# Kernel optimization log

Hardware: AMD Instinct MI355X
Metric: run time of the kernel (lower is better)

The kernel has to match this reference:

```python
import jax, jax.numpy as jnp
import numpy as np

X_CH, Y_CH = 3, 31
C = X_CH + Y_CH            # s_channels = m_channels = 34
A = C * (C - 1) // 2       # 561 Givens rotation angles
SMIN, SMAX = 0.001, 1000.0


def setup_inputs() -> dict:
    key = jax.random.key(0)
    k1, k2 = jax.random.split(key)
    x = jax.random.normal(k1, (4, X_CH, 64, 64), dtype=jnp.float32)
    W = jax.random.normal(k2, (C + C + A, X_CH), dtype=jnp.float32) * 0.1
    b = jnp.zeros((C + C + A,), dtype=jnp.float32)
    return {"x": x, "W": W, "b": b}


def _covariance(s, a):
    # s: (B, C, H, W) positive variances; a: (B, A, H, W) rotation angles.
    B, _, H, Wd = s.shape
    cs = jnp.moveaxis(jnp.cos(a), 1, 0)  # (A, B, H, W)
    ss = jnp.moveaxis(jnp.sin(a), 1, 0)  # (A, B, H, W)
    ii, jj = np.triu_indices(C, k=1)      # same (i, j) order as the torch double loop
    ii = jnp.asarray(ii, dtype=jnp.int32)
    jj = jnp.asarray(jj, dtype=jnp.int32)

    # R starts as identity; each Givens rotation rij only mixes columns i and j
    # of R (R <- R @ rij), so we update two columns instead of a full matmul.
    R0 = jnp.broadcast_to(jnp.eye(C, dtype=s.dtype), (B, H, Wd, C, C))

    def step(R, inp):
        c_, s_, i, j = inp
        col_i = R[..., i]                      # (B, H, W, C)
        col_j = R[..., j]
        c_ = c_[..., None]
        s_ = s_[..., None]
        R = R.at[..., i].set(c_ * col_i + s_ * col_j)
        R = R.at[..., j].set(-s_ * col_i + c_ * col_j)
        return R, None

    R, _ = jax.lax.scan(step, R0, (cs, ss, ii, jj))
    sp = jnp.transpose(s, (0, 2, 3, 1))        # (B, H, W, C)
    # S = R^T D R with D = diag(sp): S[k,n] = sum_m R[m,k] * sp[m] * R[m,n]
    S = jnp.einsum('bhwmk,bhwm,bhwmn->bhwkn', R, sp, R)
    D = jnp.zeros((B, H, Wd, C, C), dtype=s.dtype).at[..., jnp.arange(C), jnp.arange(C)].set(sp)
    return S, R, D


def reference(x, W, b):
    # 1x1-conv encoder: (B, 3, H, W) -> (B, 629, H, W)
    w = jnp.einsum('oc,bchw->bohw', W, x) + b[None, :, None, None]
    m = jnp.transpose(w[:, :C], (0, 2, 3, 1))                  # (B, H, W, C) mean
    s = jax.nn.sigmoid(w[:, C:2 * C])
    s = SMIN * (1.0 - s) + SMAX * s                            # (B, C, H, W)
    a = jnp.pi * jnp.tanh(w[:, 2 * C:])                        # (B, A, H, W)
    S, _, _ = _covariance(s, a)
    return m, S, s
```

## Files before the change

### kernel.cpp

```cpp
#include <hip/hip_runtime.h>


#define CCH 34
#define ACH 561
#define HWPIX 4096
#define NPIX 16384
#define PXB 6
#define NPRB 3
#define NTHR 128
#define CSPP (141 * 16)
#define CBUF (NPRB * CSPP)
#define VROW 36
#define VPX (17 * VROW * 4)
#define OFF_S 557056
#define OFF_s 19496960
#define LOG2E 1.4426950408889634f

typedef float    f32x2 __attribute__((ext_vector_type(2)));
typedef _Float16 h2    __attribute__((ext_vector_type(2)));

struct Pairs {
    short i[ACH]; short j[ACH];
    constexpr Pairs() : i(), j() {
        int p = 0;
        for (int a = 0; a < CCH - 1; ++a)
            for (int b = a + 1; b < CCH; ++b) { i[p] = (short)a; j[p] = (short)b; ++p; }
    }
};
__device__ constexpr Pairs PR{};

__device__ __forceinline__ float dot2h(h2 a, h2 b, float c) {
#if __has_builtin(__builtin_amdgcn_fdot2)
    return __builtin_amdgcn_fdot2(a, b, c, false);
#else
    return fmaf((float)a[0], (float)b[0], fmaf((float)a[1], (float)b[1], c));
#endif
}

__device__ __forceinline__ void rot2(f32x2& Ri, f32x2& Rj, f32x2 c2, f32x2 s2) {
    f32x2 t1 = s2 * Rj;
    f32x2 t2 = s2 * Ri;
    Ri = __builtin_elementwise_fma(c2, Ri, t1);
    Rj = __builtin_elementwise_fma(c2, Rj, -t2);
}

template <int P0, int P1>
__device__ __forceinline__ void apply_rots(f32x2* R2, const f32x2* cs2) {
    #pragma unroll
    for (int k = P0; k < P1; ++k) {
        f32x2 c2 = cs2[2 * (k - P0)];
        f32x2 s2 = cs2[2 * (k - P0) + 1];
        rot2(R2[PR.i[k]], R2[PR.j[k]], c2, s2);
    }
}

__device__ __forceinline__ float2 cs_of(float wv) {
    float e  = __builtin_amdgcn_exp2f((2.0f * LOG2E) * wv);
    float tt = 1.0f - 2.0f * __builtin_amdgcn_rcpf(e + 1.0f);
    float rv = 0.5f * tt;
    return make_float2(__builtin_amdgcn_cosf(rv), __builtin_amdgcn_sinf(rv));
}

template <int G0, int LEN>
__device__ __forceinline__ void fill_cs(const float* __restrict__ Wm,
                                        const float* __restrict__ bvec,
                                        const float* xs, char* buf,
                                        int npr, int t) {
    for (int o = t; o < npr * LEN; o += NTHR) {
        int pr = (int)((unsigned)o / (unsigned)LEN);
        int l  = o - pr * LEN;
        int ch = 2 * CCH + G0 + l;
        float w0 = Wm[ch * 3 + 0], w1 = Wm[ch * 3 + 1], w2 = Wm[ch * 3 + 2];
        float bb = bvec[ch];
        int pa = 2 * pr, pb = 2 * pr + 1;
        float2 A = cs_of(fmaf(w0, xs[pa*3+0], fmaf(w1, xs[pa*3+1], w2 * xs[pa*3+2])) + bb);
        float2 B = cs_of(fmaf(w0, xs[pb*3+0], fmaf(w1, xs[pb*3+1], w2 * xs[pb*3+2])) + bb);
        float4 cell; cell.x = A.x; cell.y = B.x; cell.z = A.y; cell.w = B.y;
        *(float4*)(buf + pr * CSPP + l * 16) = cell;
    }
}

__global__ __launch_bounds__(NTHR, 2) void gpd_kernel(
    const float* __restrict__ x,
    const float* __restrict__ Wm,
    const float* __restrict__ bvec,
    float* __restrict__ out)
{
    __shared__ alignas(16) char cbuf[2 * CBUF];
    __shared__ _Float16 lds_sh[PXB * CCH];
    __shared__ float xs[PXB * 3];

    const int t   = threadIdx.x;
    const int p0  = blockIdx.x * PXB;
    const int npx = min(PXB, NPIX - p0);
    const int npr = npx >> 1;

    for (int i = t; i < npx * 3; i += NTHR) {
        int px = (int)((unsigned)i / 3u); int c = i - px * 3;
        int p = p0 + px; int b = p >> 12; int hw = p & 4095;
        xs[i] = x[(b * 3 + c) * HWPIX + hw];
    }
    __syncthreads();

    for (int o = t; o < npx * 68; o += NTHR) {
        int q = (int)((unsigned)o / 68u); int ch = o - q * 68;
        int p = p0 + q; int b = p >> 12; int hw = p & 4095;
        float wv = fmaf(Wm[ch*3+0], xs[q*3+0],
                   fmaf(Wm[ch*3+1], xs[q*3+1], Wm[ch*3+2] * xs[q*3+2])) + bvec[ch];
        if (ch < CCH) {
            out[(size_t)p * CCH + ch] = wv;
        } else {
            float e  = __builtin_amdgcn_exp2f(-wv * LOG2E);
            float sg = __builtin_amdgcn_rcpf(1.0f + e);
            float sv = fmaf(999.999f, sg, 0.001f);
            int c = ch - CCH;
            out[OFF_s + (size_t)(b * CCH + c) * HWPIX + hw] = sv;
            lds_sh[q * CCH + c] = (_Float16)sv;
        }
    }

    const int pr = t / CCH;
    const int m  = t - pr * CCH;
    const bool act = (t < npr * CCH);

    f32x2 R2[CCH];
    #pragma unroll
    for (int k = 0; k < CCH; ++k) { R2[k][0] = (k == m) ? 1.0f : 0.0f; R2[k][1] = R2[k][0]; }

    const f32x2* rp0 = (const f32x2*)(cbuf + pr * CSPP);
    const f32x2* rp1 = (const f32x2*)(cbuf + CBUF + pr * CSPP);

    fill_cs<0, 141>(Wm, bvec, xs, cbuf, npr, t);
    __syncthreads();

    fill_cs<141, 140>(Wm, bvec, xs, cbuf + CBUF, npr, t);
    if (act) apply_rots<0, 141>(R2, rp0);
    __syncthreads();

    fill_cs<281, 140>(Wm, bvec, xs, cbuf, npr, t);
    if (act) apply_rots<141, 281>(R2, rp1);
    __syncthreads();

    fill_cs<421, 140>(Wm, bvec, xs, cbuf + CBUF, npr, t);
    if (act) apply_rots<281, 421>(R2, rp0);
    __syncthreads();

    if (act) apply_rots<421, 561>(R2, rp1);
    __syncthreads();

    h2 Rh[CCH];
    #pragma unroll
    for (int n = 0; n < CCH; ++n) {
#if __has_builtin(__builtin_amdgcn_cvt_pkrtz)
        Rh[n] = __builtin_bit_cast(h2, __builtin_amdgcn_cvt_pkrtz(R2[n][0], R2[n][1]));
#else
        h2 hv; hv[0] = (_Float16)R2[n][0]; hv[1] = (_Float16)R2[n][1]; Rh[n] = hv;
#endif
    }

    #pragma unroll
    for (int h = 0; h < 2; ++h) {
        if (act) {
            char* base = cbuf + pr * VPX + (m >> 1) * (VROW * 4) + (m & 1) * 2;
            #pragma unroll
            for (int n = 0; n < CCH; ++n)
                *(_Float16*)(base + n * 4) = Rh[n][h];
        }
        __syncthreads();

        if (act) {
            const int px = 2 * pr + h;
            const unsigned* vb = (const unsigned*)(cbuf + pr * VPX);
            const _Float16* sh = lds_sh + px * CCH;
            float acc[CCH];
            #pragma unroll
            for (int n = 0; n < CCH; ++n) acc[n] = 0.0f;
            for (int mp = 0; mp < 17; ++mp) {
                const unsigned* row = vb + mp * VROW;
                h2 vk = __builtin_bit_cast(h2, row[m]) * *(const h2*)(sh + 2 * mp);
                #pragma unroll
                for (int g = 0; g < 8; ++g) {
                    uint4 rr = *(const uint4*)(row + 4 * g);
                    acc[4*g+0] = dot2h(vk, __builtin_bit_cast(h2, rr.x), acc[4*g+0]);
                    acc[4*g+1] = dot2h(vk, __builtin_bit_cast(h2, rr.y), acc[4*g+1]);
                    acc[4*g+2] = dot2h(vk, __builtin_bit_cast(h2, rr.z), acc[4*g+2]);
                    acc[4*g+3] = dot2h(vk, __builtin_bit_cast(h2, rr.w), acc[4*g+3]);
                }
                uint2 rr2 = *(const uint2*)(row + 32);
                acc[32] = dot2h(vk, __builtin_bit_cast(h2, rr2.x), acc[32]);
                acc[33] = dot2h(vk, __builtin_bit_cast(h2, rr2.y), acc[33]);
            }
            float* os = out + OFF_S + (size_t)(p0 + px) * (CCH * CCH) + m * CCH;
            #pragma unroll
            for (int n2 = 0; n2 < 17; ++n2) {
                float2 v; v.x = acc[2*n2]; v.y = acc[2*n2+1];
                *(float2*)(os + 2 * n2) = v;
            }
        }
        __syncthreads();
    }
}

extern "C" void kernel_launch(void* const* d_in, const int* in_sizes, int n_in,
                              void* d_out, int out_size, void* d_ws, size_t ws_size,
                              hipStream_t stream) {
    const float* x  = (const float*)d_in[0];
    const float* W  = (const float*)d_in[1];
    const float* bv = (const float*)d_in[2];
    float* out = (float*)d_out;
    const int nblk = (NPIX + PXB - 1) / PXB;
    hipLaunchKernelGGL(gpd_kernel, dim3(nblk), dim3(NTHR), 0, stream,
                       x, W, bv, out);
}
```

Baseline: 74.73 us.

## Remap threads to one pixel with two R columns each, seven pixels per block

```diff
diff --git a/kernel.cpp b/kernel.cpp
--- a/kernel.cpp
+++ b/kernel.cpp
@@ -5,11 +5,10 @@
 #define ACH 561
 #define HWPIX 4096
 #define NPIX 16384
-#define PXB 6
-#define NPRB 3
+#define PXB 7
 #define NTHR 128
-#define CSPP (141 * 16)
-#define CBUF (NPRB * CSPP)
+#define CLEN 141
+#define CSPX (CLEN * 8)
 #define VROW 36
 #define VPX (17 * VROW * 4)
 #define OFF_S 557056
@@ -45,11 +44,12 @@
 }
 
 template <int P0, int P1>
-__device__ __forceinline__ void apply_rots(f32x2* R2, const f32x2* cs2) {
+__device__ __forceinline__ void apply_rots(f32x2* R2, const char* csb) {
     #pragma unroll
     for (int k = P0; k < P1; ++k) {
-        f32x2 c2 = cs2[2 * (k - P0)];
-        f32x2 s2 = cs2[2 * (k - P0) + 1];
+        f32x2 cell = *(const f32x2*)(csb + (k - P0) * 8);
+        f32x2 c2 = __builtin_shufflevector(cell, cell, 0, 0);
+        f32x2 s2 = __builtin_shufflevector(cell, cell, 1, 1);
         rot2(R2[PR.i[k]], R2[PR.j[k]], c2, s2);
     }
 }
@@ -64,36 +64,31 @@
 template <int G0, int LEN>
 __device__ __forceinline__ void fill_cs(const float* __restrict__ Wm,
                                         const float* __restrict__ bvec,
-                                        const float* xs, char* buf,
-                                        int npr, int t) {
-    for (int o = t; o < npr * LEN; o += NTHR) {
-        int pr = (int)((unsigned)o / (unsigned)LEN);
-        int l  = o - pr * LEN;
+                                        const float* xs, char* csbuf,
+                                        int npx, int t) {
+    for (int o = t; o < npx * LEN; o += NTHR) {
+        int px = (int)((unsigned)o / (unsigned)LEN);
+        int l  = o - px * LEN;
         int ch = 2 * CCH + G0 + l;
-        float w0 = Wm[ch * 3 + 0], w1 = Wm[ch * 3 + 1], w2 = Wm[ch * 3 + 2];
-        float bb = bvec[ch];
-        int pa = 2 * pr, pb = 2 * pr + 1;
-        float2 A = cs_of(fmaf(w0, xs[pa*3+0], fmaf(w1, xs[pa*3+1], w2 * xs[pa*3+2])) + bb);
-        float2 B = cs_of(fmaf(w0, xs[pb*3+0], fmaf(w1, xs[pb*3+1], w2 * xs[pb*3+2])) + bb);
-        float4 cell; cell.x = A.x; cell.y = B.x; cell.z = A.y; cell.w = B.y;
-        *(float4*)(buf + pr * CSPP + l * 16) = cell;
-    }
-}
-
-__global__ __launch_bounds__(NTHR, 2) void gpd_kernel(
+        float wv = fmaf(Wm[ch*3+0], xs[px*3+0],
+                   fmaf(Wm[ch*3+1], xs[px*3+1], Wm[ch*3+2] * xs[px*3+2])) + bvec[ch];
+        *(float2*)(csbuf + px * CSPX + l * 8) = cs_of(wv);
+    }
+}
+
+__global__ __launch_bounds__(NTHR, 4) void gpd_kernel(
     const float* __restrict__ x,
     const float* __restrict__ Wm,
     const float* __restrict__ bvec,
     float* __restrict__ out)
 {
-    __shared__ alignas(16) char cbuf[2 * CBUF];
+    __shared__ alignas(16) char vbuf[PXB * VPX];
     __shared__ _Float16 lds_sh[PXB * CCH];
     __shared__ float xs[PXB * 3];
 
     const int t   = threadIdx.x;
     const int p0  = blockIdx.x * PXB;
     const int npx = min(PXB, NPIX - p0);
-    const int npr = npx >> 1;
 
     for (int i = t; i < npx * 3; i += NTHR) {
         int px = (int)((unsigned)i / 3u); int c = i - px * 3;
@@ -119,85 +114,80 @@
         }
     }
 
-    const int pr = t / CCH;
-    const int m  = t - pr * CCH;
-    const bool act = (t < npr * CCH);
+    const int px = t / 17;
+    const int u  = t - px * 17;
+    const bool act = (px < npx);
+    const char* csb = vbuf + px * CSPX;
 
     f32x2 R2[CCH];
     #pragma unroll
-    for (int k = 0; k < CCH; ++k) { R2[k][0] = (k == m) ? 1.0f : 0.0f; R2[k][1] = R2[k][0]; }
-
-    const f32x2* rp0 = (const f32x2*)(cbuf + pr * CSPP);
-    const f32x2* rp1 = (const f32x2*)(cbuf + CBUF + pr * CSPP);
-
-    fill_cs<0, 141>(Wm, bvec, xs, cbuf, npr, t);
-    __syncthreads();
-
-    fill_cs<141, 140>(Wm, bvec, xs, cbuf + CBUF, npr, t);
-    if (act) apply_rots<0, 141>(R2, rp0);
-    __syncthreads();
-
-    fill_cs<281, 140>(Wm, bvec, xs, cbuf, npr, t);
-    if (act) apply_rots<141, 281>(R2, rp1);
-    __syncthreads();
-
-    fill_cs<421, 140>(Wm, bvec, xs, cbuf + CBUF, npr, t);
-    if (act) apply_rots<281, 421>(R2, rp0);
-    __syncthreads();
-
-    if (act) apply_rots<421, 561>(R2, rp1);
-    __syncthreads();
-
-    h2 Rh[CCH];
-    #pragma unroll
     for (int n = 0; n < CCH; ++n) {
-#if __has_builtin(__builtin_amdgcn_cvt_pkrtz)
-        Rh[n] = __builtin_bit_cast(h2, __builtin_amdgcn_cvt_pkrtz(R2[n][0], R2[n][1]));
-#else
-        h2 hv; hv[0] = (_Float16)R2[n][0]; hv[1] = (_Float16)R2[n][1]; Rh[n] = hv;
-#endif
-    }
-
-    #pragma unroll
-    for (int h = 0; h < 2; ++h) {
-        if (act) {
-            char* base = cbuf + pr * VPX + (m >> 1) * (VROW * 4) + (m & 1) * 2;
+        R2[n][0] = (n == 2 * u)     ? 1.0f : 0.0f;
+        R2[n][1] = (n == 2 * u + 1) ? 1.0f : 0.0f;
+    }
+
+    fill_cs<0, 141>(Wm, bvec, xs, vbuf, npx, t);
+    __syncthreads();
+    if (act) apply_rots<0, 141>(R2, csb);
+    __syncthreads();
+    fill_cs<141, 140>(Wm, bvec, xs, vbuf, npx, t);
+    __syncthreads();
+    if (act) apply_rots<141, 281>(R2, csb);
+    __syncthreads();
+    fill_cs<281, 140>(Wm, bvec, xs, vbuf, npx, t);
+    __syncthreads();
+    if (act) apply_rots<281, 421>(R2, csb);
+    __syncthreads();
+    fill_cs<421, 140>(Wm, bvec, xs, vbuf, npx, t);
+    __syncthreads();
+    if (act) apply_rots<421, 561>(R2, csb);
+    __syncthreads();
+
+    if (act) {
+        unsigned* vb = (unsigned*)(vbuf + px * VPX) + u * VROW;
+        #pragma unroll
+        for (int n = 0; n < CCH; ++n)
+            vb[n] = __builtin_bit_cast(unsigned,
+                        __builtin_amdgcn_cvt_pkrtz(R2[n][0], R2[n][1]));
+    }
+    __syncthreads();
+
+    if (act) {
+        const unsigned* vb = (const unsigned*)(vbuf + px * VPX);
+        const _Float16* sh = lds_sh + px * CCH;
+        float aL[CCH], aH[CCH];
+        #pragma unroll
+        for (int n = 0; n < CCH; ++n) { aL[n] = 0.0f; aH[n] = 0.0f; }
+        for (int mp = 0; mp < 17; ++mp) {
+            const unsigned* row = vb + mp * VROW;
+            h2 sh2 = *(const h2*)(sh + 2 * mp);
+            h2 vkL = __builtin_bit_cast(h2, row[2 * u])     * sh2;
+            h2 vkH = __builtin_bit_cast(h2, row[2 * u + 1]) * sh2;
             #pragma unroll
-            for (int n = 0; n < CCH; ++n)
-                *(_Float16*)(base + n * 4) = Rh[n][h];
+            for (int g = 0; g < 8; ++g) {
+                uint4 rr = *(const uint4*)(row + 4 * g);
+                h2 r0 = __builtin_bit_cast(h2, rr.x), r1 = __builtin_bit_cast(h2, rr.y);
+                h2 r2 = __builtin_bit_cast(h2, rr.z), r3 = __builtin_bit_cast(h2, rr.w);
+                aL[4*g+0] = dot2h(vkL, r0, aL[4*g+0]);  aH[4*g+0] = dot2h(vkH, r0, aH[4*g+0]);
+                aL[4*g+1] = dot2h(vkL, r1, aL[4*g+1]);  aH[4*g+1] = dot2h(vkH, r1, aH[4*g+1]);
+                aL[4*g+2] = dot2h(vkL, r2, aL[4*g+2]);  aH[4*g+2] = dot2h(vkH, r2, aH[4*g+2]);
+                aL[4*g+3] = dot2h(vkL, r3, aL[4*g+3]);  aH[4*g+3] = dot2h(vkH, r3, aH[4*g+3]);
+            }
+            uint2 rr2 = *(const uint2*)(row + 32);
+            h2 r32 = __builtin_bit_cast(h2, rr2.x), r33 = __builtin_bit_cast(h2, rr2.y);
+            aL[32] = dot2h(vkL, r32, aL[32]);  aH[32] = dot2h(vkH, r32, aH[32]);
+            aL[33] = dot2h(vkL, r33, aL[33]);  aH[33] = dot2h(vkH, r33, aH[33]);
         }
-        __syncthreads();
-
-        if (act) {
-            const int px = 2 * pr + h;
-            const unsigned* vb = (const unsigned*)(cbuf + pr * VPX);
-            const _Float16* sh = lds_sh + px * CCH;
-            float acc[CCH];
-            #pragma unroll
-            for (int n = 0; n < CCH; ++n) acc[n] = 0.0f;
-            for (int mp = 0; mp < 17; ++mp) {
-                const unsigned* row = vb + mp * VROW;
-                h2 vk = __builtin_bit_cast(h2, row[m]) * *(const h2*)(sh + 2 * mp);
-                #pragma unroll
-                for (int g = 0; g < 8; ++g) {
-                    uint4 rr = *(const uint4*)(row + 4 * g);
-                    acc[4*g+0] = dot2h(vk, __builtin_bit_cast(h2, rr.x), acc[4*g+0]);
-                    acc[4*g+1] = dot2h(vk, __builtin_bit_cast(h2, rr.y), acc[4*g+1]);
-                    acc[4*g+2] = dot2h(vk, __builtin_bit_cast(h2, rr.z), acc[4*g+2]);
-                    acc[4*g+3] = dot2h(vk, __builtin_bit_cast(h2, rr.w), acc[4*g+3]);
-                }
-                uint2 rr2 = *(const uint2*)(row + 32);
-                acc[32] = dot2h(vk, __builtin_bit_cast(h2, rr2.x), acc[32]);
-                acc[33] = dot2h(vk, __builtin_bit_cast(h2, rr2.y), acc[33]);
-            }
-            float* os = out + OFF_S + (size_t)(p0 + px) * (CCH * CCH) + m * CCH;
-            #pragma unroll
-            for (int n2 = 0; n2 < 17; ++n2) {
-                float2 v; v.x = acc[2*n2]; v.y = acc[2*n2+1];
-                *(float2*)(os + 2 * n2) = v;
-            }
+        float* os = out + OFF_S + (size_t)(p0 + px) * (CCH * CCH) + 2 * u * CCH;
+        #pragma unroll
+        for (int q = 0; q < 17; ++q) {
+            float4 v;
+            v.x = (4*q+0 < 34) ? aL[4*q+0] : aH[4*q+0-34];
+            v.y = (4*q+1 < 34) ? aL[4*q+1] : aH[4*q+1-34];
+            v.z = (4*q+2 < 34) ? aL[4*q+2] : aH[4*q+2-34];
+            v.w = (4*q+3 < 34) ? aL[4*q+3] : aH[4*q+3-34];
+            *(float4*)(os + 4 * q) = v;
         }
-        __syncthreads();
     }
 }
 
```

New measurement: 74.74 us. Within noise of the previous version (+0.0%).
